# Kernel tuning notes

Measured on AMD Instinct MI355X. Metric: run time of the kernel, lower is better.

The kernel has to match this reference:

```python
import jax, jax.numpy as jnp
import numpy as np

H = 8  # num_heads
EPS = 1e-5


def layer_norm(x, g, b):
    mu = jnp.mean(x, axis=-1, keepdims=True)
    var = jnp.mean((x - mu) ** 2, axis=-1, keepdims=True)
    return (x - mu) * jax.lax.rsqrt(var + EPS) * g + b


def setup_inputs() -> dict:
    key = jax.random.key(0)
    ks = jax.random.split(key, 8)
    B, N, C = 2, 2048, 512
    Dff = 2048
    s = 0.02
    x = jax.random.normal(ks[0], (B, N, C), dtype=jnp.float32)
    mask = (jax.random.uniform(ks[1], (N, N)) > 0.5).astype(jnp.float32)
    return {
        "x": x,
        "mask": mask,
        "w_qkv": jax.random.normal(ks[2], (3 * C, C), dtype=jnp.float32) * s,
        "w_proj": jax.random.normal(ks[3], (C, C), dtype=jnp.float32) * s,
        "b_proj": jnp.zeros((C,), jnp.float32),
        "g1": jnp.ones((C,), jnp.float32),
        "beta1": jnp.zeros((C,), jnp.float32),
        "g2": jnp.ones((C,), jnp.float32),
        "beta2": jnp.zeros((C,), jnp.float32),
        "w1": jax.random.normal(ks[4], (Dff, C), dtype=jnp.float32) * s,
        "bm1": jnp.zeros((Dff,), jnp.float32),
        "w2": jax.random.normal(ks[5], (C, Dff), dtype=jnp.float32) * s,
        "bm2": jnp.zeros((C,), jnp.float32),
    }


def attn_block(h, mask, w_qkv, w_proj, b_proj):
    B, N, C = h.shape
    hd = C // H
    scale = hd ** -0.5
    qkv = (h @ w_qkv.T).reshape(B, N, 3, H, hd)
    q, k, v = jnp.moveaxis(qkv, 2, 0)          # each [B, N, H, hd]
    q = q.transpose(0, 2, 1, 3)                 # [B, H, N, hd]
    k = k.transpose(0, 2, 1, 3)
    v = v.transpose(0, 2, 1, 3)
    attn = jnp.einsum("bhnd,bhmd->bhnm", q, k) * scale
    attn = attn * mask                          # multiplicative sparse mask
    attn = jax.nn.softmax(attn, axis=-1)
    o = jnp.einsum("bhnm,bhmd->bhnd", attn, v)
    o = o.transpose(0, 2, 1, 3).reshape(B, N, C)
    return o @ w_proj.T + b_proj


def reference(x, mask, w_qkv, w_proj, b_proj, g1, beta1, g2, beta2, w1, bm1, w2, bm2):
    # pre-norm transformer block, dropout/drop_path disabled (eval)
    y = x + attn_block(layer_norm(x, g1, beta1), mask, w_qkv, w_proj, b_proj)
    h = layer_norm(y, g2, beta2)
    h = jax.nn.gelu(h @ w1.T + bm1, approximate=False)  # torch F.gelu default (erf)
    z = y + (h @ w2.T + bm2)
    return z
```

## Files before the change

### kernel.cpp

```cpp
#include <hip/hip_runtime.h>
#include <cmath>
#include <stdint.h>

#define N_SEQ 2048
#define C_DIM 512
#define BATCH 2
#define NHEAD 8
#define DFF   2048
#define M_ROWS (BATCH * N_SEQ)

typedef unsigned short ushort_t;
typedef unsigned long long u64;
typedef __bf16 bf16x8 __attribute__((ext_vector_type(8)));
typedef float  f32x4  __attribute__((ext_vector_type(4)));
typedef float  f32x16 __attribute__((ext_vector_type(16)));

__device__ __forceinline__ float bf2f(ushort_t u) {
    union { unsigned int i; float f; } v; v.i = ((unsigned int)u) << 16; return v.f;
}
__device__ __forceinline__ ushort_t f2bf_(float f) {
    union { float f; unsigned int i; } v; v.f = f;
    unsigned int r = v.i + 0x7fffu + ((v.i >> 16) & 1u);
    return (ushort_t)(r >> 16);
}

__device__ __forceinline__ void load_lds16(const ushort_t* g, ushort_t* lds_wave_base) {
    __builtin_amdgcn_global_load_lds(
        (const __attribute__((address_space(1))) void*)g,
        (__attribute__((address_space(3))) void*)lds_wave_base, 16, 0, 0);
}

__global__ void probe_kernel(const unsigned int* __restrict__ g1w, int* __restrict__ flag) {
    if (threadIdx.x == 0 && blockIdx.x == 0)
        *flag = (g1w[0] == 0x3F800000u) ? 1 : 0;
}

__global__ __launch_bounds__(256) void convert_kernel(const int* __restrict__ flag,
        const void* w_qkv, const void* w_proj, const void* w1, const void* w2,
        ushort_t* wq_bf, ushort_t* wp_bf, ushort_t* w1_bf, ushort_t* w2_bf) {
    long e = ((long)blockIdx.x * 256 + threadIdx.x) * 8;
    const void* src; ushort_t* dst; long off;
    if      (e < 786432)  { src = w_qkv; dst = wq_bf;  off = e; }
    else if (e < 1048576) { src = w_proj; dst = wp_bf; off = e - 786432; }
    else if (e < 2097152) { src = w1;    dst = w1_bf;  off = e - 1048576; }
    else                  { src = w2;    dst = w2_bf;  off = e - 2097152; }
    bf16x8 r;
    if (*flag) {
        const float4* q = (const float4*)((const float*)src + off);
        float4 a = q[0], b = q[1];
        r[0]=(__bf16)a.x; r[1]=(__bf16)a.y; r[2]=(__bf16)a.z; r[3]=(__bf16)a.w;
        r[4]=(__bf16)b.x; r[5]=(__bf16)b.y; r[6]=(__bf16)b.z; r[7]=(__bf16)b.w;
    } else {
        r = *(const bf16x8*)((const ushort_t*)src + off);
    }
    *(bf16x8*)(dst + off) = r;
}

__global__ __launch_bounds__(256) void maskpack_kernel(const int* __restrict__ flag,
        const void* __restrict__ mask, u64* __restrict__ maskT) {
    int key = blockIdx.x * 256 + threadIdx.x;
    int qw  = blockIdx.y;
    int is32 = *flag;
    u64 bits = 0;
    for (int j = 0; j < 64; ++j) {
        bool m = is32 ? (((const float*)mask)[(size_t)(qw * 64 + j) * N_SEQ + key] != 0.0f)
                      : ((((const ushort_t*)mask)[(size_t)(qw * 64 + j) * N_SEQ + key] & 0x7fffu) != 0);
        bits |= (u64)m << j;
    }
    maskT[(size_t)key * 32 + qw] = bits;
}

template <typename TX, typename TG>
__device__ __forceinline__ void ln_body(const TX* __restrict__ x, const TG* __restrict__ g,
                                        const TG* __restrict__ b, ushort_t* __restrict__ out) {
    int row  = blockIdx.x * 4 + (threadIdx.x >> 6);
    int lane = threadIdx.x & 63;
    const TX* xr = x + (size_t)row * C_DIM + lane * 8;
    float v[8];
    if (sizeof(TX) == 2) {
        bf16x8 t = *(const bf16x8*)xr;
        #pragma unroll
        for (int j = 0; j < 8; ++j) v[j] = (float)t[j];
    } else {
        const float4* q = (const float4*)xr;
        float4 a = q[0], c = q[1];
        v[0]=a.x; v[1]=a.y; v[2]=a.z; v[3]=a.w; v[4]=c.x; v[5]=c.y; v[6]=c.z; v[7]=c.w;
    }
    float s = 0.f, sq = 0.f;
    #pragma unroll
    for (int j = 0; j < 8; ++j) { s += v[j]; sq += v[j] * v[j]; }
    #pragma unroll
    for (int m = 1; m < 64; m <<= 1) { s += __shfl_xor(s, m, 64); sq += __shfl_xor(sq, m, 64); }
    float mean = s * (1.0f / C_DIM);
    float var  = fmaxf(sq * (1.0f / C_DIM) - mean * mean, 0.0f);
    float rs = rsqrtf(var + 1e-5f);
    float gv[8], bv[8];
    const TG* gp = g + lane * 8; const TG* bp = b + lane * 8;
    if (sizeof(TG) == 2) {
        bf16x8 tg = *(const bf16x8*)gp, tb = *(const bf16x8*)bp;
        #pragma unroll
        for (int j = 0; j < 8; ++j) { gv[j] = (float)tg[j]; bv[j] = (float)tb[j]; }
    } else {
        const float4* qg = (const float4*)gp; const float4* qb = (const float4*)bp;
        float4 a=qg[0], c=qg[1], d=qb[0], e=qb[1];
        gv[0]=a.x;gv[1]=a.y;gv[2]=a.z;gv[3]=a.w;gv[4]=c.x;gv[5]=c.y;gv[6]=c.z;gv[7]=c.w;
        bv[0]=d.x;bv[1]=d.y;bv[2]=d.z;bv[3]=d.w;bv[4]=e.x;bv[5]=e.y;bv[6]=e.z;bv[7]=e.w;
    }
    bf16x8 o;
    #pragma unroll
    for (int j = 0; j < 8; ++j) o[j] = (__bf16)((v[j] - mean) * rs * gv[j] + bv[j]);
    *(bf16x8*)(out + (size_t)row * C_DIM + lane * 8) = o;
}

__global__ __launch_bounds__(256) void ln1_kernel(const int* __restrict__ flag, const void* x,
                                                  const void* g, const void* b, ushort_t* out) {
    if (*flag) ln_body<float, float>((const float*)x, (const float*)g, (const float*)b, out);
    else       ln_body<ushort_t, ushort_t>((const ushort_t*)x, (const ushort_t*)g, (const ushort_t*)b, out);
}
__global__ __launch_bounds__(256) void ln2_kernel(const int* __restrict__ flag, const ushort_t* y,
                                                  const void* g, const void* b, ushort_t* out) {
    if (*flag) ln_body<ushort_t, float>(y, (const float*)g, (const float*)b, out);
    else       ln_body<ushort_t, ushort_t>(y, (const ushort_t*)g, (const ushort_t*)b, out);
}

template <int BM, int K, bool HAS_BIAS, int ACT, int RES_MODE, int OUT_MODE>
__global__ __launch_bounds__(256) void gemm_kernel(const int* __restrict__ flag,
        const ushort_t* __restrict__ A, const ushort_t* __restrict__ W,
        const void* __restrict__ bias, const void* __restrict__ res,
        void* __restrict__ Cout, int Nout) {
    constexpr int MT = BM / 32;
    __shared__ __align__(16) ushort_t As[2][BM][32];
    __shared__ __align__(16) ushort_t Bs[2][64][32];
    int t = threadIdx.x;
    int wave = t >> 6, lane = t & 63, quad = lane >> 4, l16 = lane & 15;
    int wave_m = wave >> 1, wave_n = wave & 1;
    int row0 = blockIdx.y * BM, col0 = blockIdx.x * 64;

    f32x4 acc[MT][2] = {};
    int arow = t >> 2, kofs = (t & 3) * 8;

    for (int k0 = 0; k0 < K; k0 += 64) {
        #pragma unroll
        for (int h = 0; h < 2; ++h) {
            load_lds16(A + (size_t)(row0 + arow) * K + k0 + h * 32 + kofs, &As[h][0][0] + wave * 512);
            if (BM == 128)
                load_lds16(A + (size_t)(row0 + 64 + arow) * K + k0 + h * 32 + kofs, &As[h][64][0] + wave * 512);
            load_lds16(W + (size_t)(col0 + arow) * K + k0 + h * 32 + kofs, &Bs[h][0][0] + wave * 512);
        }
        __syncthreads();
        #pragma unroll
        for (int h = 0; h < 2; ++h) {
            bf16x8 af[MT], bfr[2];
            #pragma unroll
            for (int i = 0; i < MT; ++i)
                af[i] = *(const bf16x8*)&As[h][wave_m * (BM / 2) + i * 16 + l16][quad * 8];
            #pragma unroll
            for (int j = 0; j < 2; ++j)
                bfr[j] = *(const bf16x8*)&Bs[h][wave_n * 32 + j * 16 + l16][quad * 8];
            #pragma unroll
            for (int i = 0; i < MT; ++i)
                #pragma unroll
                for (int j = 0; j < 2; ++j)
                    acc[i][j] = __builtin_amdgcn_mfma_f32_16x16x32_bf16(af[i], bfr[j], acc[i][j], 0, 0, 0);
        }
        __syncthreads();
    }

    int is32 = *flag;
    #pragma unroll
    for (int j = 0; j < 2; ++j) {
        int col = col0 + wave_n * 32 + j * 16 + l16;
        float bv = 0.0f;
        if (HAS_BIAS) bv = is32 ? ((const float*)bias)[col] : bf2f(((const ushort_t*)bias)[col]);
        #pragma unroll
        for (int i = 0; i < MT; ++i) {
            #pragma unroll
            for (int r = 0; r < 4; ++r) {
                int row = row0 + wave_m * (BM / 2) + i * 16 + quad * 4 + r;
                float v = acc[i][j][r] + bv;
                if (ACT == 1) v = 0.5f * v * (1.0f + erff(v * 0.70710678118654752f));
                size_t idx = (size_t)row * Nout + col;
                if (RES_MODE == 1) v += is32 ? ((const float*)res)[idx] : bf2f(((const ushort_t*)res)[idx]);
                if (RES_MODE == 3) v += bf2f(((const ushort_t*)res)[idx]);
                if (OUT_MODE == 0) ((ushort_t*)Cout)[idx] = f2bf_(v);
                else { if (is32) ((float*)Cout)[idx] = v; else ((ushort_t*)Cout)[idx] = f2bf_(v); }
            }
        }
    }
}

__global__ __launch_bounds__(128, 3) void attn_kernel(const int* __restrict__ flag,
        const ushort_t* __restrict__ qkv, const u64* __restrict__ maskT,
        ushort_t* __restrict__ Opart, float* __restrict__ Lpart) {
    __shared__ __align__(16) ushort_t Ks[64][64];
    __shared__ __align__(16) ushort_t VTs[64][68];
    __shared__ __align__(16) ushort_t Ps[2][32][68];
    int t = threadIdx.x;
    int wave = t >> 6, lane = t & 63, l32 = lane & 31, half = lane >> 5;
    int qtile = blockIdx.x, bh = blockIdx.y, sp = blockIdx.z;
    int b = bh >> 3, h = bh & 7;
    int qbase = qtile * 64;

    const ushort_t* base = qkv + (size_t)b * N_SEQ * 1536;
    const ushort_t* qp = base + h * 64;
    const ushort_t* kp = base + 512 + h * 64;
    const ushort_t* vp = base + 1024 + h * 64;

    bf16x8 aq[4];
    int qrow = qbase + wave * 32 + l32;
    #pragma unroll
    for (int c = 0; c < 4; ++c)
        aq[c] = *(const bf16x8*)(qp + (size_t)qrow * 1536 + c * 16 + half * 8);

    f32x16 o_acc[2] = {};
    float lsum[16] = {};
    const float scale = 0.125f;

    int v_kp[2], v_db[2];
    #pragma unroll
    for (int s = 0; s < 2; ++s) {
        int idx = s * 128 + t;
        v_kp[s] = (idx & 31) * 2;
        v_db[s] = (idx >> 5) * 8;
    }
    const int n_base = sp * 512;
    bf16x8 vreg[2][2];
    #pragma unroll
    for (int s = 0; s < 2; ++s)
        #pragma unroll
        for (int u = 0; u < 2; ++u)
            vreg[s][u] = *(const bf16x8*)(vp + (size_t)(n_base + v_kp[s] + u) * 1536 + v_db[s]);
    u64 mw[2];
    #pragma unroll
    for (int t2 = 0; t2 < 2; ++t2)
        mw[t2] = maskT[(size_t)(n_base + t2 * 32 + l32) * 32 + qtile];

    for (int i = 0; i < 8; ++i) {
        int n0 = n_base + i * 64;
        __syncthreads();
        #pragma unroll
        for (int s = 0; s < 4; ++s)
            load_lds16(kp + (size_t)(n0 + (s * 2 + wave) * 8 + (lane >> 3)) * 1536 + (lane & 7) * 8,
                       &Ks[(s * 2 + wave) * 8][0]);
        #pragma unroll
        for (int s = 0; s < 2; ++s)
            #pragma unroll
            for (int j = 0; j < 8; ++j) {
                unsigned int pair = (unsigned int)__builtin_bit_cast(unsigned short, vreg[s][0][j])
                                  | ((unsigned int)__builtin_bit_cast(unsigned short, vreg[s][1][j]) << 16);
                *(unsigned int*)&VTs[v_db[s] + j][v_kp[s]] = pair;
            }
        __syncthreads();
        if (i < 7) {
            int n1 = n0 + 64;
            #pragma unroll
            for (int s = 0; s < 2; ++s)
                #pragma unroll
                for (int u = 0; u < 2; ++u)
                    vreg[s][u] = *(const bf16x8*)(vp + (size_t)(n1 + v_kp[s] + u) * 1536 + v_db[s]);
        }
        f32x16 s_acc[2] = {};
        #pragma unroll
        for (int t2 = 0; t2 < 2; ++t2)
            #pragma unroll
            for (int c = 0; c < 4; ++c) {
                bf16x8 bk = *(const bf16x8*)&Ks[t2 * 32 + l32][c * 16 + half * 8];
                s_acc[t2] = __builtin_amdgcn_mfma_f32_32x32x16_bf16(aq[c], bk, s_acc[t2], 0, 0, 0);
            }
        #pragma unroll
        for (int t2 = 0; t2 < 2; ++t2)
            #pragma unroll
            for (int r = 0; r < 16; ++r) {
                int row_local = (r & 3) + 8 * (r >> 2) + 4 * half;
                float e = __expf(s_acc[t2][r] * scale);
                float p = ((mw[t2] >> (wave * 32 + row_local)) & 1) ? e : 1.0f;
                lsum[r] += p;
                Ps[wave][row_local][t2 * 32 + l32] = __builtin_bit_cast(unsigned short, (__bf16)p);
            }
        if (i < 7) {
            #pragma unroll
            for (int t2 = 0; t2 < 2; ++t2)
                mw[t2] = maskT[(size_t)(n0 + 64 + t2 * 32 + l32) * 32 + qtile];
        }
        bf16x8 pf[4];
        #pragma unroll
        for (int kc = 0; kc < 4; ++kc)
            pf[kc] = *(const bf16x8*)&Ps[wave][l32][kc * 16 + half * 8];
        #pragma unroll
        for (int dt = 0; dt < 2; ++dt)
            #pragma unroll
            for (int kc = 0; kc < 4; ++kc) {
                bf16x8 bv = *(const bf16x8*)&VTs[dt * 32 + l32][kc * 16 + half * 8];
                o_acc[dt] = __builtin_amdgcn_mfma_f32_32x32x16_bf16(pf[kc], bv, o_acc[dt], 0, 0, 0);
            }
    }
    #pragma unroll
    for (int m = 1; m < 32; m <<= 1)
        #pragma unroll
        for (int r = 0; r < 16; ++r) lsum[r] += __shfl_xor(lsum[r], m, 64);
    ushort_t* op = Opart + (size_t)(sp * 16 + bh) * N_SEQ * 64;
    #pragma unroll
    for (int r = 0; r < 16; ++r) {
        int row_local = (r & 3) + 8 * (r >> 2) + 4 * half;
        int q = qbase + wave * 32 + row_local;
        #pragma unroll
        for (int dt = 0; dt < 2; ++dt)
            op[(size_t)q * 64 + dt * 32 + l32] = f2bf_(o_acc[dt][r]);
        if (l32 == 0)
            Lpart[(size_t)(sp * 16 + bh) * N_SEQ + q] = lsum[r];
    }
}

__global__ __launch_bounds__(256) void combine_kernel(const ushort_t* __restrict__ Opart,
        const float* __restrict__ Lpart, ushort_t* __restrict__ attno) {
    int gid = blockIdx.x * 256 + threadIdx.x;
    int rowg = gid >> 4;
    int dq = (gid & 15) * 4;
    int bh = rowg >> 11, q = rowg & 2047, b = bh >> 3, h = bh & 7;
    const size_t SP = (size_t)16 * N_SEQ * 64;
    float acc[4] = {};
    float l = 0.0f;
    #pragma unroll
    for (int sp = 0; sp < 4; ++sp) {
        ushort4 o = *(const ushort4*)&Opart[sp * SP + (size_t)rowg * 64 + dq];
        acc[0] += bf2f(o.x); acc[1] += bf2f(o.y); acc[2] += bf2f(o.z); acc[3] += bf2f(o.w);
        l += Lpart[(size_t)sp * 16 * N_SEQ + rowg];
    }
    float inv = 1.0f / l;
    ushort4 res;
    res.x = f2bf_(acc[0] * inv); res.y = f2bf_(acc[1] * inv);
    res.z = f2bf_(acc[2] * inv); res.w = f2bf_(acc[3] * inv);
    *(ushort4*)&attno[((size_t)b * N_SEQ + q) * C_DIM + h * 64 + dq] = res;
}

extern "C" void kernel_launch(void* const* d_in, const int* in_sizes, int n_in,
                              void* d_out, int out_size, void* d_ws, size_t ws_size,
                              hipStream_t stream) {
    char* ws = (char*)d_ws;
    const size_t KB = 1024;
    int*      flag  = (int*)ws;
    ushort_t* wq_bf = (ushort_t*)(ws + 256 * KB);
    ushort_t* wp_bf = (ushort_t*)(ws + 1792 * KB);
    ushort_t* w1_bf = (ushort_t*)(ws + 2304 * KB);
    ushort_t* w2_bf = (ushort_t*)(ws + 4352 * KB);
    u64*      maskT = (u64*)     (ws + 6400 * KB);
    ushort_t* h     = (ushort_t*)(ws + 6912 * KB);
    ushort_t* attno = (ushort_t*)(ws + 11008 * KB);
    ushort_t* qkv   = (ushort_t*)(ws + 15104 * KB);
    ushort_t* Opart = (ushort_t*)(ws + 27392 * KB);
    float*    Lpart = (float*)   (ws + 43776 * KB);
    ushort_t* y     = (ushort_t*)(ws + 27392 * KB);
    ushort_t* gmid  = (ushort_t*)(ws + 11008 * KB);

    probe_kernel<<<1, 64, 0, stream>>>((const unsigned int*)d_in[5], flag);
    convert_kernel<<<1536, 256, 0, stream>>>(flag, d_in[2], d_in[3], d_in[9], d_in[11],
                                             wq_bf, wp_bf, w1_bf, w2_bf);
    maskpack_kernel<<<dim3(8, 32), 256, 0, stream>>>(flag, d_in[1], maskT);
    ln1_kernel<<<M_ROWS / 4, 256, 0, stream>>>(flag, d_in[0], d_in[5], d_in[6], h);
    gemm_kernel<128, 512, false, 0, 0, 0><<<dim3(1536 / 64, 32), 256, 0, stream>>>(
        flag, h, wq_bf, nullptr, nullptr, qkv, 1536);
    attn_kernel<<<dim3(N_SEQ / 64, BATCH * NHEAD, 4), 128, 0, stream>>>(flag, qkv, maskT, Opart, Lpart);
    combine_kernel<<<2048, 256, 0, stream>>>(Opart, Lpart, attno);
    gemm_kernel<64, 512, true, 0, 1, 0><<<dim3(C_DIM / 64, 64), 256, 0, stream>>>(
        flag, attno, wp_bf, d_in[4], d_in[0], y, C_DIM);
    ln2_kernel<<<M_ROWS / 4, 256, 0, stream>>>(flag, y, d_in[7], d_in[8], h);
    gemm_kernel<128, 512, true, 1, 0, 0><<<dim3(DFF / 64, 32), 256, 0, stream>>>(
        flag, h, w1_bf, d_in[10], nullptr, gmid, DFF);
    gemm_kernel<64, 2048, true, 0, 3, 2><<<dim3(C_DIM / 64, 64), 256, 0, stream>>>(
        flag, gmid, w2_bf, d_in[12], y, d_out, C_DIM);
}
```

Measured before the change: 295.7 us.

## Rework attention to transposed S=K·Q with register P shuffle, retile GEMMs

The attention kernel now computes K·Qᵀ, so each lane owns one query row. Probabilities stay in registers and are exchanged with cross-half shuffles instead of going through an LDS P buffer, and row sums become a single scalar per lane. K tiles are staged through registers with a padded LDS layout, and the mask is repacked row-major per query. The GEMM kernel is retiled to 64-row by BN-column tiles with a K-step of 32 and one barrier pair per step, and workspace buffers are rearranged so the split outputs alias existing buffers. The 32-wide K step doubles the number of barriers per GEMM.

```diff
diff --git a/kernel.cpp b/kernel.cpp
--- a/kernel.cpp
+++ b/kernel.cpp
@@ -22,6 +22,9 @@
     union { float f; unsigned int i; } v; v.f = f;
     unsigned int r = v.i + 0x7fffu + ((v.i >> 16) & 1u);
     return (ushort_t)(r >> 16);
+}
+__device__ __forceinline__ unsigned short bfbits(float f) {
+    return __builtin_bit_cast(unsigned short, (__bf16)f);
 }
 
 __device__ __forceinline__ void load_lds16(const ushort_t* g, ushort_t* lds_wave_base) {
@@ -57,17 +60,18 @@
 }
 
 __global__ __launch_bounds__(256) void maskpack_kernel(const int* __restrict__ flag,
-        const void* __restrict__ mask, u64* __restrict__ maskT) {
-    int key = blockIdx.x * 256 + threadIdx.x;
-    int qw  = blockIdx.y;
+        const void* __restrict__ mask, u64* __restrict__ maskM) {
+    int id = blockIdx.x * 256 + threadIdx.x;
+    int q = id >> 5, kb = id & 31;
     int is32 = *flag;
+    size_t base = (size_t)q * N_SEQ + kb * 64;
     u64 bits = 0;
     for (int j = 0; j < 64; ++j) {
-        bool m = is32 ? (((const float*)mask)[(size_t)(qw * 64 + j) * N_SEQ + key] != 0.0f)
-                      : ((((const ushort_t*)mask)[(size_t)(qw * 64 + j) * N_SEQ + key] & 0x7fffu) != 0);
+        bool m = is32 ? (((const float*)mask)[base + j] != 0.0f)
+                      : ((((const ushort_t*)mask)[base + j] & 0x7fffu) != 0);
         bits |= (u64)m << j;
     }
-    maskT[(size_t)key * 32 + qw] = bits;
+    maskM[(size_t)q * 32 + kb] = bits;
 }
 
 template <typename TX, typename TG>
@@ -123,60 +127,56 @@
     else       ln_body<ushort_t, ushort_t>(y, (const ushort_t*)g, (const ushort_t*)b, out);
 }
 
-template <int BM, int K, bool HAS_BIAS, int ACT, int RES_MODE, int OUT_MODE>
+template <int BN, int K, bool HAS_BIAS, int ACT, int RES_MODE, int OUT_MODE>
 __global__ __launch_bounds__(256) void gemm_kernel(const int* __restrict__ flag,
         const ushort_t* __restrict__ A, const ushort_t* __restrict__ W,
         const void* __restrict__ bias, const void* __restrict__ res,
         void* __restrict__ Cout, int Nout) {
-    constexpr int MT = BM / 32;
-    __shared__ __align__(16) ushort_t As[2][BM][32];
-    __shared__ __align__(16) ushort_t Bs[2][64][32];
+    constexpr int MT  = (BN == 128) ? 2 : 1;
+    constexpr int RPW = (BN == 128) ? 32 : 16;
+    __shared__ __align__(16) ushort_t As[64 * 32];
+    __shared__ __align__(16) ushort_t Bs[BN * 32];
     int t = threadIdx.x;
     int wave = t >> 6, lane = t & 63, quad = lane >> 4, l16 = lane & 15;
-    int wave_m = wave >> 1, wave_n = wave & 1;
-    int row0 = blockIdx.y * BM, col0 = blockIdx.x * 64;
-
-    f32x4 acc[MT][2] = {};
+    int wm = (BN == 128) ? (wave >> 1) : wave;
+    int wn = (BN == 128) ? (wave & 1) : 0;
+    int row0 = blockIdx.y * 64, col0 = blockIdx.x * BN;
+
+    f32x4 acc[MT][4] = {};
     int arow = t >> 2, kofs = (t & 3) * 8;
 
-    for (int k0 = 0; k0 < K; k0 += 64) {
-        #pragma unroll
-        for (int h = 0; h < 2; ++h) {
-            load_lds16(A + (size_t)(row0 + arow) * K + k0 + h * 32 + kofs, &As[h][0][0] + wave * 512);
-            if (BM == 128)
-                load_lds16(A + (size_t)(row0 + 64 + arow) * K + k0 + h * 32 + kofs, &As[h][64][0] + wave * 512);
-            load_lds16(W + (size_t)(col0 + arow) * K + k0 + h * 32 + kofs, &Bs[h][0][0] + wave * 512);
-        }
+    for (int k0 = 0; k0 < K; k0 += 32) {
+        load_lds16(A + (size_t)(row0 + arow) * K + k0 + kofs, As + wave * 512);
+        load_lds16(W + (size_t)(col0 + arow) * K + k0 + kofs, Bs + wave * 512);
+        if (BN == 128)
+            load_lds16(W + (size_t)(col0 + 64 + arow) * K + k0 + kofs, Bs + 2048 + wave * 512);
         __syncthreads();
-        #pragma unroll
-        for (int h = 0; h < 2; ++h) {
-            bf16x8 af[MT], bfr[2];
-            #pragma unroll
-            for (int i = 0; i < MT; ++i)
-                af[i] = *(const bf16x8*)&As[h][wave_m * (BM / 2) + i * 16 + l16][quad * 8];
-            #pragma unroll
-            for (int j = 0; j < 2; ++j)
-                bfr[j] = *(const bf16x8*)&Bs[h][wave_n * 32 + j * 16 + l16][quad * 8];
-            #pragma unroll
-            for (int i = 0; i < MT; ++i)
-                #pragma unroll
-                for (int j = 0; j < 2; ++j)
-                    acc[i][j] = __builtin_amdgcn_mfma_f32_16x16x32_bf16(af[i], bfr[j], acc[i][j], 0, 0, 0);
-        }
+        bf16x8 af[MT], bfr[4];
+        #pragma unroll
+        for (int i = 0; i < MT; ++i)
+            af[i] = *(const bf16x8*)&As[(wm * RPW + i * 16 + l16) * 32 + quad * 8];
+        #pragma unroll
+        for (int j = 0; j < 4; ++j)
+            bfr[j] = *(const bf16x8*)&Bs[(wn * 64 + j * 16 + l16) * 32 + quad * 8];
+        #pragma unroll
+        for (int i = 0; i < MT; ++i)
+            #pragma unroll
+            for (int j = 0; j < 4; ++j)
+                acc[i][j] = __builtin_amdgcn_mfma_f32_16x16x32_bf16(af[i], bfr[j], acc[i][j], 0, 0, 0);
         __syncthreads();
     }
 
     int is32 = *flag;
     #pragma unroll
-    for (int j = 0; j < 2; ++j) {
-        int col = col0 + wave_n * 32 + j * 16 + l16;
+    for (int j = 0; j < 4; ++j) {
+        int col = col0 + wn * 64 + j * 16 + l16;
         float bv = 0.0f;
         if (HAS_BIAS) bv = is32 ? ((const float*)bias)[col] : bf2f(((const ushort_t*)bias)[col]);
         #pragma unroll
         for (int i = 0; i < MT; ++i) {
             #pragma unroll
             for (int r = 0; r < 4; ++r) {
-                int row = row0 + wave_m * (BM / 2) + i * 16 + quad * 4 + r;
+                int row = row0 + wm * RPW + i * 16 + quad * 4 + r;
                 float v = acc[i][j][r] + bv;
                 if (ACT == 1) v = 0.5f * v * (1.0f + erff(v * 0.70710678118654752f));
                 size_t idx = (size_t)row * Nout + col;
@@ -189,140 +189,160 @@
     }
 }
 
-__global__ __launch_bounds__(128, 3) void attn_kernel(const int* __restrict__ flag,
-        const ushort_t* __restrict__ qkv, const u64* __restrict__ maskT,
-        ushort_t* __restrict__ Opart, float* __restrict__ Lpart) {
-    __shared__ __align__(16) ushort_t Ks[64][64];
+__global__ __launch_bounds__(128) void attn_kernel(
+        const ushort_t* __restrict__ qkv, const u64* __restrict__ maskM,
+        ushort_t* __restrict__ o0, ushort_t* __restrict__ o1,
+        ushort_t* __restrict__ o2, ushort_t* __restrict__ o3,
+        float* __restrict__ Lpart) {
+    __shared__ __align__(16) ushort_t Ks[64][68];
     __shared__ __align__(16) ushort_t VTs[64][68];
-    __shared__ __align__(16) ushort_t Ps[2][32][68];
     int t = threadIdx.x;
-    int wave = t >> 6, lane = t & 63, l32 = lane & 31, half = lane >> 5;
+    int wave = t >> 6, lane = t & 63, l32 = lane & 31, H = lane >> 5;
     int qtile = blockIdx.x, bh = blockIdx.y, sp = blockIdx.z;
     int b = bh >> 3, h = bh & 7;
-    int qbase = qtile * 64;
+    int q = qtile * 64 + wave * 32 + l32;
 
     const ushort_t* base = qkv + (size_t)b * N_SEQ * 1536;
     const ushort_t* qp = base + h * 64;
     const ushort_t* kp = base + 512 + h * 64;
     const ushort_t* vp = base + 1024 + h * 64;
 
-    bf16x8 aq[4];
-    int qrow = qbase + wave * 32 + l32;
+    bf16x8 bQ[4];
     #pragma unroll
     for (int c = 0; c < 4; ++c)
-        aq[c] = *(const bf16x8*)(qp + (size_t)qrow * 1536 + c * 16 + half * 8);
+        bQ[c] = *(const bf16x8*)(qp + (size_t)q * 1536 + c * 16 + H * 8);
+
+    int k_row = (t >> 3);
+    int k_ch  = (t & 7) * 8;
+    int v_kp0 = (t & 31) * 2;
+    int v_db0 = (t >> 5) * 8;
+    const int n_base = sp * 512;
+
+    bf16x8 kreg[4], vreg[2][2];
+    #pragma unroll
+    for (int s = 0; s < 4; ++s)
+        kreg[s] = *(const bf16x8*)(kp + (size_t)(n_base + s * 16 + k_row) * 1536 + k_ch);
+    #pragma unroll
+    for (int s = 0; s < 2; ++s)
+        #pragma unroll
+        for (int u = 0; u < 2; ++u)
+            vreg[s][u] = *(const bf16x8*)(vp + (size_t)(n_base + v_kp0 + u) * 1536 + v_db0 + s * 32);
+    u64 mw = maskM[(size_t)q * 32 + (n_base >> 6)];
 
     f32x16 o_acc[2] = {};
-    float lsum[16] = {};
+    float lsum = 0.0f;
     const float scale = 0.125f;
-
-    int v_kp[2], v_db[2];
-    #pragma unroll
-    for (int s = 0; s < 2; ++s) {
-        int idx = s * 128 + t;
-        v_kp[s] = (idx & 31) * 2;
-        v_db[s] = (idx >> 5) * 8;
-    }
-    const int n_base = sp * 512;
-    bf16x8 vreg[2][2];
-    #pragma unroll
-    for (int s = 0; s < 2; ++s)
-        #pragma unroll
-        for (int u = 0; u < 2; ++u)
-            vreg[s][u] = *(const bf16x8*)(vp + (size_t)(n_base + v_kp[s] + u) * 1536 + v_db[s]);
-    u64 mw[2];
-    #pragma unroll
-    for (int t2 = 0; t2 < 2; ++t2)
-        mw[t2] = maskT[(size_t)(n_base + t2 * 32 + l32) * 32 + qtile];
 
     for (int i = 0; i < 8; ++i) {
         int n0 = n_base + i * 64;
         __syncthreads();
         #pragma unroll
         for (int s = 0; s < 4; ++s)
-            load_lds16(kp + (size_t)(n0 + (s * 2 + wave) * 8 + (lane >> 3)) * 1536 + (lane & 7) * 8,
-                       &Ks[(s * 2 + wave) * 8][0]);
+            *(bf16x8*)&Ks[s * 16 + k_row][k_ch] = kreg[s];
         #pragma unroll
         for (int s = 0; s < 2; ++s)
             #pragma unroll
             for (int j = 0; j < 8; ++j) {
                 unsigned int pair = (unsigned int)__builtin_bit_cast(unsigned short, vreg[s][0][j])
                                   | ((unsigned int)__builtin_bit_cast(unsigned short, vreg[s][1][j]) << 16);
-                *(unsigned int*)&VTs[v_db[s] + j][v_kp[s]] = pair;
+                *(unsigned int*)&VTs[v_db0 + s * 32 + j][v_kp0] = pair;
             }
         __syncthreads();
         if (i < 7) {
             int n1 = n0 + 64;
             #pragma unroll
+            for (int s = 0; s < 4; ++s)
+                kreg[s] = *(const bf16x8*)(kp + (size_t)(n1 + s * 16 + k_row) * 1536 + k_ch);
+            #pragma unroll
             for (int s = 0; s < 2; ++s)
                 #pragma unroll
                 for (int u = 0; u < 2; ++u)
-                    vreg[s][u] = *(const bf16x8*)(vp + (size_t)(n1 + v_kp[s] + u) * 1536 + v_db[s]);
+                    vreg[s][u] = *(const bf16x8*)(vp + (size_t)(n1 + v_kp0 + u) * 1536 + v_db0 + s * 32);
         }
         f32x16 s_acc[2] = {};
         #pragma unroll
-        for (int t2 = 0; t2 < 2; ++t2)
+        for (int kt = 0; kt < 2; ++kt)
             #pragma unroll
             for (int c = 0; c < 4; ++c) {
-                bf16x8 bk = *(const bf16x8*)&Ks[t2 * 32 + l32][c * 16 + half * 8];
-                s_acc[t2] = __builtin_amdgcn_mfma_f32_32x32x16_bf16(aq[c], bk, s_acc[t2], 0, 0, 0);
-            }
-        #pragma unroll
-        for (int t2 = 0; t2 < 2; ++t2)
+                bf16x8 aK = *(const bf16x8*)&Ks[kt * 32 + l32][c * 16 + H * 8];
+                s_acc[kt] = __builtin_amdgcn_mfma_f32_32x32x16_bf16(aK, bQ[c], s_acc[kt], 0, 0, 0);
+            }
+        unsigned int P2[2][8];
+        #pragma unroll
+        for (int kt = 0; kt < 2; ++kt) {
+            float p[16];
             #pragma unroll
             for (int r = 0; r < 16; ++r) {
-                int row_local = (r & 3) + 8 * (r >> 2) + 4 * half;
-                float e = __expf(s_acc[t2][r] * scale);
-                float p = ((mw[t2] >> (wave * 32 + row_local)) & 1) ? e : 1.0f;
-                lsum[r] += p;
-                Ps[wave][row_local][t2 * 32 + l32] = __builtin_bit_cast(unsigned short, (__bf16)p);
-            }
-        if (i < 7) {
-            #pragma unroll
-            for (int t2 = 0; t2 < 2; ++t2)
-                mw[t2] = maskT[(size_t)(n0 + 64 + t2 * 32 + l32) * 32 + qtile];
-        }
-        bf16x8 pf[4];
-        #pragma unroll
-        for (int kc = 0; kc < 4; ++kc)
-            pf[kc] = *(const bf16x8*)&Ps[wave][l32][kc * 16 + half * 8];
-        #pragma unroll
-        for (int dt = 0; dt < 2; ++dt)
-            #pragma unroll
-            for (int kc = 0; kc < 4; ++kc) {
-                bf16x8 bv = *(const bf16x8*)&VTs[dt * 32 + l32][kc * 16 + half * 8];
-                o_acc[dt] = __builtin_amdgcn_mfma_f32_32x32x16_bf16(pf[kc], bv, o_acc[dt], 0, 0, 0);
-            }
-    }
-    #pragma unroll
-    for (int m = 1; m < 32; m <<= 1)
-        #pragma unroll
-        for (int r = 0; r < 16; ++r) lsum[r] += __shfl_xor(lsum[r], m, 64);
-    ushort_t* op = Opart + (size_t)(sp * 16 + bh) * N_SEQ * 64;
-    #pragma unroll
-    for (int r = 0; r < 16; ++r) {
-        int row_local = (r & 3) + 8 * (r >> 2) + 4 * half;
-        int q = qbase + wave * 32 + row_local;
-        #pragma unroll
-        for (int dt = 0; dt < 2; ++dt)
-            op[(size_t)q * 64 + dt * 32 + l32] = f2bf_(o_acc[dt][r]);
-        if (l32 == 0)
-            Lpart[(size_t)(sp * 16 + bh) * N_SEQ + q] = lsum[r];
-    }
-}
-
-__global__ __launch_bounds__(256) void combine_kernel(const ushort_t* __restrict__ Opart,
+                int keyloc = kt * 32 + (r & 3) + 8 * (r >> 2) + 4 * H;
+                float e = __expf(s_acc[kt][r] * scale);
+                p[r] = ((mw >> keyloc) & 1) ? e : 1.0f;
+                lsum += p[r];
+            }
+            #pragma unroll
+            for (int pr = 0; pr < 8; ++pr)
+                P2[kt][pr] = (unsigned int)bfbits(p[2 * pr])
+                           | ((unsigned int)bfbits(p[2 * pr + 1]) << 16);
+        }
+        if (i < 7) mw = maskM[(size_t)q * 32 + ((n0 + 64) >> 6)];
+        unsigned int rv[2][4];
+        #pragma unroll
+        for (int kt = 0; kt < 2; ++kt)
+            #pragma unroll
+            for (int u = 0; u < 4; ++u) {
+                int idx = (u & 1) + (u >> 1) * 4;
+                unsigned int send = H ? P2[kt][idx] : P2[kt][idx + 2];
+                rv[kt][u] = (unsigned int)__shfl_xor((int)send, 32, 64);
+            }
+        #pragma unroll
+        for (int kc = 0; kc < 4; ++kc) {
+            const int kt = kc >> 1, klo = kc & 1;
+            union { unsigned int w[4]; bf16x8 v; } bP;
+            #pragma unroll
+            for (int w = 0; w < 4; ++w) {
+                unsigned int own = H ? P2[kt][(w & 1) + 4 * klo + 2] : P2[kt][(w & 1) + 4 * klo];
+                unsigned int oth = rv[kt][(w & 1) + 2 * klo];
+                bP.w[w] = ((w >> 1) == H) ? own : oth;
+            }
+            #pragma unroll
+            for (int dt = 0; dt < 2; ++dt) {
+                bf16x8 aV = *(const bf16x8*)&VTs[dt * 32 + l32][kc * 16 + H * 8];
+                o_acc[dt] = __builtin_amdgcn_mfma_f32_32x32x16_bf16(aV, bP.v, o_acc[dt], 0, 0, 0);
+            }
+        }
+    }
+    lsum += __shfl_xor(lsum, 32, 64);
+    ushort_t* osel = (sp == 0) ? o0 : (sp == 1) ? o1 : (sp == 2) ? o2 : o3;
+    ushort_t* op = osel + (size_t)bh * N_SEQ * 64;
+    #pragma unroll
+    for (int dt = 0; dt < 2; ++dt)
+        #pragma unroll
+        for (int r4 = 0; r4 < 4; ++r4) {
+            int d = dt * 32 + 8 * r4 + 4 * H;
+            ushort4 val;
+            val.x = f2bf_(o_acc[dt][r4 * 4 + 0]);
+            val.y = f2bf_(o_acc[dt][r4 * 4 + 1]);
+            val.z = f2bf_(o_acc[dt][r4 * 4 + 2]);
+            val.w = f2bf_(o_acc[dt][r4 * 4 + 3]);
+            *(ushort4*)&op[(size_t)q * 64 + d] = val;
+        }
+    if (H == 0)
+        Lpart[((size_t)sp * 16 + bh) * N_SEQ + q] = lsum;
+}
+
+__global__ __launch_bounds__(256) void combine_kernel(
+        const ushort_t* __restrict__ o0, const ushort_t* __restrict__ o1,
+        const ushort_t* __restrict__ o2, const ushort_t* __restrict__ o3,
         const float* __restrict__ Lpart, ushort_t* __restrict__ attno) {
     int gid = blockIdx.x * 256 + threadIdx.x;
     int rowg = gid >> 4;
     int dq = (gid & 15) * 4;
-    int bh = rowg >> 11, q = rowg & 2047, b = bh >> 3, h = bh & 7;
-    const size_t SP = (size_t)16 * N_SEQ * 64;
+    int bh = rowg >> 11, qq = rowg & 2047, b = bh >> 3, h = bh & 7;
+    const ushort_t* ops[4] = { o0, o1, o2, o3 };
     float acc[4] = {};
     float l = 0.0f;
     #pragma unroll
     for (int sp = 0; sp < 4; ++sp) {
-        ushort4 o = *(const ushort4*)&Opart[sp * SP + (size_t)rowg * 64 + dq];
+        ushort4 o = *(const ushort4*)&ops[sp][(size_t)rowg * 64 + dq];
         acc[0] += bf2f(o.x); acc[1] += bf2f(o.y); acc[2] += bf2f(o.z); acc[3] += bf2f(o.w);
         l += Lpart[(size_t)sp * 16 * N_SEQ + rowg];
     }
@@ -330,7 +350,7 @@
     ushort4 res;
     res.x = f2bf_(acc[0] * inv); res.y = f2bf_(acc[1] * inv);
     res.z = f2bf_(acc[2] * inv); res.w = f2bf_(acc[3] * inv);
-    *(ushort4*)&attno[((size_t)b * N_SEQ + q) * C_DIM + h * 64 + dq] = res;
+    *(ushort4*)&attno[((size_t)b * N_SEQ + qq) * C_DIM + h * 64 + dq] = res;
 }
 
 extern "C" void kernel_launch(void* const* d_in, const int* in_sizes, int n_in,
@@ -343,28 +363,32 @@
     ushort_t* wp_bf = (ushort_t*)(ws + 1792 * KB);
     ushort_t* w1_bf = (ushort_t*)(ws + 2304 * KB);
     ushort_t* w2_bf = (ushort_t*)(ws + 4352 * KB);
-    u64*      maskT = (u64*)     (ws + 6400 * KB);
+    u64*      maskM = (u64*)     (ws + 6400 * KB);
     ushort_t* h     = (ushort_t*)(ws + 6912 * KB);
     ushort_t* attno = (ushort_t*)(ws + 11008 * KB);
-    ushort_t* qkv   = (ushort_t*)(ws + 15104 * KB);
-    ushort_t* Opart = (ushort_t*)(ws + 27392 * KB);
-    float*    Lpart = (float*)   (ws + 43776 * KB);
-    ushort_t* y     = (ushort_t*)(ws + 27392 * KB);
-    ushort_t* gmid  = (ushort_t*)(ws + 11008 * KB);
+    ushort_t* y     = (ushort_t*)(ws + 15104 * KB);
+    ushort_t* qkv   = (ushort_t*)(ws + 19200 * KB);
+    ushort_t* Op2   = (ushort_t*)(ws + 31488 * KB);
+    ushort_t* Op3   = (ushort_t*)(ws + 35584 * KB);
+    float*    Lpart = (float*)   (ws + 39680 * KB);
+    ushort_t* Op0   = h;
+    ushort_t* Op1   = y;
+    ushort_t* gmid  = (ushort_t*)(ws + 19200 * KB);
 
     probe_kernel<<<1, 64, 0, stream>>>((const unsigned int*)d_in[5], flag);
     convert_kernel<<<1536, 256, 0, stream>>>(flag, d_in[2], d_in[3], d_in[9], d_in[11],
                                              wq_bf, wp_bf, w1_bf, w2_bf);
-    maskpack_kernel<<<dim3(8, 32), 256, 0, stream>>>(flag, d_in[1], maskT);
+    maskpack_kernel<<<256, 256, 0, stream>>>(flag, d_in[1], maskM);
     ln1_kernel<<<M_ROWS / 4, 256, 0, stream>>>(flag, d_in[0], d_in[5], d_in[6], h);
-    gemm_kernel<128, 512, false, 0, 0, 0><<<dim3(1536 / 64, 32), 256, 0, stream>>>(
+    gemm_kernel<128, 512, false, 0, 0, 0><<<dim3(1536 / 128, 64), 256, 0, stream>>>(
         flag, h, wq_bf, nullptr, nullptr, qkv, 1536);
-    attn_kernel<<<dim3(N_SEQ / 64, BATCH * NHEAD, 4), 128, 0, stream>>>(flag, qkv, maskT, Opart, Lpart);
-    combine_kernel<<<2048, 256, 0, stream>>>(Opart, Lpart, attno);
+    attn_kernel<<<dim3(N_SEQ / 64, BATCH * NHEAD, 4), 128, 0, stream>>>(
+        qkv, maskM, Op0, Op1, Op2, Op3, Lpart);
+    combine_kernel<<<2048, 256, 0, stream>>>(Op0, Op1, Op2, Op3, Lpart, attno);
     gemm_kernel<64, 512, true, 0, 1, 0><<<dim3(C_DIM / 64, 64), 256, 0, stream>>>(
         flag, attno, wp_bf, d_in[4], d_in[0], y, C_DIM);
     ln2_kernel<<<M_ROWS / 4, 256, 0, stream>>>(flag, y, d_in[7], d_in[8], h);
-    gemm_kernel<128, 512, true, 1, 0, 0><<<dim3(DFF / 64, 32), 256, 0, stream>>>(
+    gemm_kernel<128, 512, true, 1, 0, 0><<<dim3(DFF / 128, 64), 256, 0, stream>>>(
         flag, h, w1_bf, d_in[10], nullptr, gmid, DFF);
     gemm_kernel<64, 2048, true, 0, 3, 2><<<dim3(C_DIM / 64, 64), 256, 0, stream>>>(
         flag, gmid, w2_bf, d_in[12], y, d_out, C_DIM);
```

Measured after the change: 263.1 us. -11.0%, faster.
